# Optimization experiments

Measured on AMD Instinct MI355X. Metric: run time of the kernel, lower is better.

## Reference

```python
import jax, jax.numpy as jnp
import numpy as np

PRE_NMS_TOPN = 6000   # cfg.TEST.RPN_PRE_NMS_TOP_N
POST_NMS_TOPN = 1000  # cfg.TEST.RPN_POST_NMS_TOP_N
NMS_THRESH = 0.7      # cfg.TEST.RPN_NMS_THRESH
MIN_SIZE = 0.0        # cfg.TEST.RPN_MIN_SIZE
BBOX_XFORM_CLIP = float(np.log(1000.0 / 16.0))
FEAT_STRIDE = 8.0     # 1 / spatial_scale


def _generate_anchors(base_size=16, ratios=(0.5, 1.0, 2.0), scales=(2, 4, 8, 16, 32)):
    """Standard Detectron anchor generation -> (A, 4) = (15, 4)."""
    def whctrs(a):
        w = a[2] - a[0] + 1.0
        h = a[3] - a[1] + 1.0
        return w, h, a[0] + 0.5 * (w - 1.0), a[1] + 0.5 * (h - 1.0)

    def mk(ws, hs, xc, yc):
        ws = ws[:, None]; hs = hs[:, None]
        return np.hstack([xc - 0.5 * (ws - 1.0), yc - 0.5 * (hs - 1.0),
                          xc + 0.5 * (ws - 1.0), yc + 0.5 * (hs - 1.0)])

    base = np.array([0.0, 0.0, base_size - 1.0, base_size - 1.0])
    w, h, xc, yc = whctrs(base)
    rs = np.array(ratios)
    ws = np.round(np.sqrt(w * h / rs))
    hs = np.round(ws * rs)
    ratio_anchors = mk(ws, hs, xc, yc)
    out = []
    for a in ratio_anchors:
        w, h, xc, yc = whctrs(a)
        sc = np.array(scales, dtype=np.float64)
        out.append(mk(w * sc, h * sc, xc, yc))
    return np.vstack(out).astype(np.float32)


def _proposals_one_image(all_anchors, im_info, bbox_deltas, scores):
    # bbox_deltas: (4A, H, W), scores: (A, H, W)
    deltas = bbox_deltas.transpose(1, 2, 0).reshape(-1, 4)  # (K*A, 4)
    s = scores.transpose(1, 2, 0).reshape(-1)               # (K*A,)

    # pre-NMS top-k by objectness (argpartition+argsort in original)
    top_s, order = jax.lax.top_k(s, PRE_NMS_TOPN)
    d = deltas[order]
    anc = all_anchors[order]

    # bbox_transform with weights (1,1,1,1) and dw/dh clipping
    ws = anc[:, 2] - anc[:, 0] + 1.0
    hs = anc[:, 3] - anc[:, 1] + 1.0
    cx = anc[:, 0] + 0.5 * ws
    cy = anc[:, 1] + 0.5 * hs
    dx, dy = d[:, 0], d[:, 1]
    dw = jnp.minimum(d[:, 2], BBOX_XFORM_CLIP)
    dh = jnp.minimum(d[:, 3], BBOX_XFORM_CLIP)
    pcx = dx * ws + cx
    pcy = dy * hs + cy
    pw = jnp.exp(dw) * ws
    ph = jnp.exp(dh) * hs
    x1 = pcx - 0.5 * pw
    y1 = pcy - 0.5 * ph
    x2 = pcx + 0.5 * pw - 1.0
    y2 = pcy + 0.5 * ph - 1.0

    # clip_tiled_boxes to image extent
    h_im, w_im, scale = im_info[0], im_info[1], im_info[2]
    x1 = jnp.clip(x1, 0.0, w_im - 1.0)
    y1 = jnp.clip(y1, 0.0, h_im - 1.0)
    x2 = jnp.clip(x2, 0.0, w_im - 1.0)
    y2 = jnp.clip(y2, 0.0, h_im - 1.0)
    boxes = jnp.stack([x1, y1, x2, y2], axis=1)  # (PRE, 4)

    # _filter_boxes -> validity mask (replaces gather-by-keep)
    bws = x2 - x1 + 1.0
    bhs = y2 - y1 + 1.0
    min_sz = MIN_SIZE * scale
    valid = (bws >= min_sz) & (bhs >= min_sz) & ((x1 + bws / 2.0) < w_im) & ((y1 + bhs / 2.0) < h_im)

    # greedy NMS on score-sorted boxes (boxes already sorted descending)
    areas = bws * bhs
    ix1 = jnp.maximum(x1[:, None], x1[None, :])
    iy1 = jnp.maximum(y1[:, None], y1[None, :])
    ix2 = jnp.minimum(x2[:, None], x2[None, :])
    iy2 = jnp.minimum(y2[:, None], y2[None, :])
    inter = jnp.maximum(ix2 - ix1 + 1.0, 0.0) * jnp.maximum(iy2 - iy1 + 1.0, 0.0)
    iou = inter / (areas[:, None] + areas[None, :] - inter)

    later = jnp.arange(PRE_NMS_TOPN)

    def body(i, keep):
        sup = keep[i] & (iou[i] > NMS_THRESH) & (later > i)
        return keep & ~sup

    keep = jax.lax.fori_loop(0, PRE_NMS_TOPN, body, valid)

    # fixed-size output: top POST_NMS_TOPN surviving boxes, padded (score=-1, box=0)
    masked = jnp.where(keep, top_s, -1.0)
    out_s, idx = jax.lax.top_k(masked, POST_NMS_TOPN)
    pad = (out_s > -1.0).astype(boxes.dtype)
    out_b = boxes[idx] * pad[:, None]
    return out_b, out_s


def reference(rpn_cls_prob, rpn_bbox_pred, im_info, anchors):
    N, A, H, W = rpn_cls_prob.shape
    dt = rpn_bbox_pred.dtype
    shift_x = jnp.arange(W, dtype=dt) * FEAT_STRIDE
    shift_y = jnp.arange(H, dtype=dt) * FEAT_STRIDE
    # torch.meshgrid default 'ij' ordering (faithful to original)
    sx, sy = jnp.meshgrid(shift_x, shift_y, indexing='ij')  # (W, H)
    shifts = jnp.stack([sx.ravel(), sy.ravel(), sx.ravel(), sy.ravel()], axis=1)  # (K, 4)
    all_anchors = (anchors[None, :, :] + shifts[:, None, :]).reshape(-1, 4)  # (K*A, 4)

    boxes, probs = jax.vmap(_proposals_one_image, in_axes=(None, 0, 0, 0))(
        all_anchors, im_info, rpn_bbox_pred, rpn_cls_prob)
    batch_inds = jnp.broadcast_to(jnp.arange(N, dtype=boxes.dtype)[:, None, None],
                                  (N, POST_NMS_TOPN, 1))
    rois = jnp.concatenate([batch_inds, boxes], axis=-1).reshape(-1, 5)
    return rois, probs.reshape(-1)


def setup_inputs() -> dict:
    key = jax.random.key(0)
    k1, k2 = jax.random.split(key)
    N, A, H, W = 2, 15, 128, 128
    rpn_cls_prob = jax.random.uniform(k1, (N, A, H, W), dtype=jnp.float32)
    rpn_bbox_pred = jax.random.normal(k2, (N, 4 * A, H, W), dtype=jnp.float32) * 0.2
    im_info = jnp.tile(jnp.array([[1024.0, 1024.0, 1.0]], dtype=jnp.float32), (N, 1))
    anchors = jnp.asarray(_generate_anchors())
    return {"rpn_cls_prob": rpn_cls_prob, "rpn_bbox_pred": rpn_bbox_pred,
            "im_info": im_info, "anchors": anchors}
```

## Files before the change

### kernel.cpp

```cpp
#include <hip/hip_runtime.h>
#include <hip/hip_bf16.h>

#define A_NUM 15
#define HDIM 128
#define WDIM 128
#define HW (HDIM*WDIM)
#define PER_IMG (A_NUM*HW)
#define NIMG 2
#define PRE_N 6000
#define POST_N 1000
#define NBLK 94
#define NPAD (NBLK*64)
#define SORTN 8192
#define CHUNK4 4096
#define NBIN 16384
#define HPART 16
#define NLOADS 47

typedef unsigned long long ull;

#define META_OFF   0u
#define HIST_OFF   64u
#define SEL_OFF    131136u
#define BOX_OFF    262208u
#define VALIDW_OFF 550976u
#define MASK_OFF   553024u

__device__ __forceinline__ unsigned int f2ord(float f) {
    unsigned int u = __float_as_uint(f);
    return (u & 0x80000000u) ? ~u : (u | 0x80000000u);
}
__device__ __forceinline__ float ord2f(unsigned int u) {
    unsigned int s = (u & 0x80000000u) ? (u ^ 0x80000000u) : ~u;
    return __uint_as_float(s);
}
__device__ __forceinline__ ull readlane64(ull v, int l) {
    unsigned int lo = (unsigned int)__builtin_amdgcn_readlane((int)(unsigned int)v, l);
    unsigned int hi = (unsigned int)__builtin_amdgcn_readlane((int)(unsigned int)(v >> 32), l);
    return ((ull)hi << 32) | lo;
}

typedef const unsigned int __attribute__((address_space(1)))* gas_u32;
typedef unsigned int __attribute__((address_space(3)))* las_u32;

__device__ __forceinline__ void async_col(const ull* __restrict__ gcol, ull* lcol, int t) {
    #pragma unroll
    for (int q = 0; q < NLOADS; ++q) {
        __builtin_amdgcn_global_load_lds(
            (gas_u32)(const void*)((const char*)gcol + q * 1024 + t * 16),
            (las_u32)(void*)((char*)lcol + q * 1024 + t * 16),
            16, 0, 0);
    }
}

__global__ __launch_bounds__(1024) void k_hist16(const float* __restrict__ cls,
                                                 unsigned int* __restrict__ hist) {
    __shared__ unsigned int h[NBIN];
    int img = blockIdx.y, part = blockIdx.x;
    int t = threadIdx.x;
    for (int b = t; b < NBIN; b += 1024) h[b] = 0;
    __syncthreads();
    int base = img * PER_IMG + part * (PER_IMG / HPART);
    for (int e = t; e < PER_IMG / HPART; e += 1024) {
        unsigned int u = f2ord(cls[base + e]);
        unsigned int bin = (u >> 16) - 0x8000u;
        if (bin > (NBIN - 1)) bin = NBIN - 1;
        atomicAdd(&h[bin], 1u);
    }
    __syncthreads();
    unsigned int* hp = hist + (size_t)img * NBIN;
    for (int b = t; b < NBIN; b += 1024)
        if (h[b]) atomicAdd(&hp[b], h[b]);
}

__global__ __launch_bounds__(1024) void k_scan16(const unsigned int* __restrict__ hist,
                                                 unsigned int* __restrict__ meta) {
    __shared__ unsigned int csum[1024];
    __shared__ unsigned int aux[64];
    __shared__ unsigned int binv[16];
    int img = blockIdx.x, t = threadIdx.x;
    const unsigned int* hp = hist + (size_t)img * NBIN;
    unsigned int s = 0;
    #pragma unroll
    for (int q = 0; q < 16; ++q) s += hp[t * 16 + q];
    csum[t] = s;
    __syncthreads();
    if (t < 64) {
        unsigned int x = 0;
        #pragma unroll
        for (int q = 0; q < 16; ++q) x += csum[t * 16 + q];
        aux[t] = x;
    }
    __syncthreads();
    if (t < 64) {
        unsigned int suf = 0;
        for (int q = t; q < 64; ++q) suf += aux[q];
        ull mb1 = __ballot(suf >= PRE_N);
        int sstar = 63 - __clzll(mb1);
        unsigned int sufnext = (unsigned)__shfl((int)suf, (sstar + 1) & 63);
        unsigned int cumAbove = (sstar == 63) ? 0u : sufnext;
        unsigned int sufC = 0;
        if (t < 16) {
            for (int q = sstar * 16 + t; q < sstar * 16 + 16; ++q) sufC += csum[q];
            sufC += cumAbove;
        }
        ull mb2 = __ballot((t < 16) && (sufC >= PRE_N));
        int crel = 63 - __clzll(mb2);
        int cstar = sstar * 16 + crel;
        unsigned int cumAbove2 = (crel == 15) ? cumAbove : (unsigned)__shfl((int)sufC, crel + 1);
        if (t < 16) binv[t] = hp[cstar * 16 + t];
        unsigned int sufB = 0;
        if (t < 16) {
            for (int q = t; q < 16; ++q) sufB += binv[q];
            sufB += cumAbove2;
        }
        ull mb3 = __ballot((t < 16) && (sufB >= PRE_N));
        int brel = 63 - __clzll(mb3);
        if (t == 0) {
            meta[2 + img] = (unsigned)(cstar * 16 + brel) + 0x8000u;
            meta[img] = 0u;
        }
    }
}

__global__ __launch_bounds__(256) void k_gather(const float* __restrict__ cls,
                                                unsigned int* __restrict__ meta,
                                                ull* __restrict__ selkeys) {
    __shared__ unsigned int lcnt[NIMG], lbase[NIMG];
    int t = threadIdx.x;
    int tid = blockIdx.x * 256 + t;
    if (t < NIMG) lcnt[t] = 0;
    __syncthreads();
    unsigned int T0 = meta[2], T1 = meta[3];
    int a = tid / HW;
    int pos = tid - a * HW;
    int m = pos * A_NUM + a;
    int lane = t & 63;
    unsigned int uv[NIMG];
    bool pr[NIMG];
    unsigned int lofs[NIMG];
    #pragma unroll
    for (int img = 0; img < NIMG; ++img) {
        unsigned int T = img ? T1 : T0;
        unsigned int u = f2ord(cls[img * PER_IMG + tid]);
        uv[img] = u;
        bool pred = (u >> 16) >= T;
        pr[img] = pred;
        ull mball = __ballot((int)pred);
        unsigned int o = 0;
        if (pred) {
            int leader = __ffsll((long long)mball) - 1;
            unsigned int wbase = 0;
            if (lane == leader) wbase = atomicAdd(&lcnt[img], (unsigned)__popcll(mball));
            wbase = (unsigned)__shfl((int)wbase, leader);
            o = wbase + (unsigned)__popcll(mball & ((1ull << lane) - 1ull));
        }
        lofs[img] = o;
    }
    __syncthreads();
    if (t < NIMG) lbase[t] = atomicAdd(&meta[t], lcnt[t]);
    __syncthreads();
    #pragma unroll
    for (int img = 0; img < NIMG; ++img) {
        if (pr[img]) {
            unsigned int p = lbase[img] + lofs[img];
            if (p < SORTN)
                selkeys[(size_t)img * SORTN + p] =
                    ((ull)(~uv[img]) << 32) | (unsigned int)m;
        }
    }
}

__global__ __launch_bounds__(512) void k_sortA(ull* __restrict__ selkeys,
                                               const unsigned int* __restrict__ meta) {
    __shared__ ull key[CHUNK4];
    int img = blockIdx.x >> 1, c = blockIdx.x & 1;
    unsigned int cnt = meta[img];
    if (cnt > SORTN) cnt = SORTN;
    ull* g = selkeys + (size_t)img * SORTN;
    int base = c * CHUNK4;
    for (int i = threadIdx.x; i < CHUNK4; i += 512)
        key[i] = (base + i < (int)cnt) ? g[base + i] : ~0ull;
    __syncthreads();
    bool desc = (c & 1);
    for (int k = 2; k <= CHUNK4; k <<= 1) {
        for (int j = k >> 1; j > 0; j >>= 1) {
            for (int p = threadIdx.x; p < CHUNK4 / 2; p += 512) {
                int i = ((p & ~(j - 1)) << 1) | (p & (j - 1));
                int x = i | j;
                bool up = (((i & k) == 0) != desc);
                ull A = key[i], B = key[x];
                if ((A > B) == up) { key[i] = B; key[x] = A; }
            }
            __syncthreads();
        }
    }
    for (int i = threadIdx.x; i < CHUNK4; i += 512) g[base + i] = key[i];
}

__global__ __launch_bounds__(512) void k_sortC(ull* __restrict__ selkeys) {
    __shared__ ull key[SORTN];
    int img = blockIdx.x;
    ull* g = selkeys + (size_t)img * SORTN;
    for (int i = threadIdx.x; i < SORTN; i += 512) key[i] = g[i];
    __syncthreads();
    for (int j = SORTN / 2; j > 0; j >>= 1) {
        for (int p = threadIdx.x; p < SORTN / 2; p += 512) {
            int i = ((p & ~(j - 1)) << 1) | (p & (j - 1));
            int x = i | j;
            ull A = key[i], B = key[x];
            if (A > B) { key[i] = B; key[x] = A; }
        }
        __syncthreads();
    }
    for (int i = threadIdx.x; i < PRE_N; i += 512) g[i] = key[i];
}

__global__ void k_decode(const ull* __restrict__ selkeys,
                         const float* __restrict__ bbox, const float* __restrict__ anchors,
                         const float* __restrict__ iminfo,
                         float* __restrict__ boxsoa, ull* __restrict__ validwArr) {
    int r = blockIdx.x * blockDim.x + threadIdx.x;
    int img = blockIdx.y;
    bool in = r < PRE_N;
    int rr = in ? r : 0;
    ull keyv = selkeys[(size_t)img * SORTN + rr];
    unsigned int m = (unsigned int)(keyv & 0xFFFFFFFFu);
    unsigned int u = ~(unsigned int)(keyv >> 32);
    float score = ord2f(u);
    int q = m / A_NUM;
    int a = m - q * A_NUM;
    int w = q & (WDIM - 1);
    int h = q >> 7;
    float sx = (float)h * 8.0f;
    float sy = (float)w * 8.0f;
    float a0 = __fadd_rn(anchors[a * 4 + 0], sx);
    float a1 = __fadd_rn(anchors[a * 4 + 1], sy);
    float a2 = __fadd_rn(anchors[a * 4 + 2], sx);
    float a3 = __fadd_rn(anchors[a * 4 + 3], sy);
    float ws = __fadd_rn(__fsub_rn(a2, a0), 1.0f);
    float hs = __fadd_rn(__fsub_rn(a3, a1), 1.0f);
    float cx = __fadd_rn(a0, __fmul_rn(0.5f, ws));
    float cy = __fadd_rn(a1, __fmul_rn(0.5f, hs));
    const float* bb = bbox + (size_t)img * 4 * A_NUM * HW;
    int base = h * WDIM + w;
    float dx = bb[(a * 4 + 0) * HW + base];
    float dy = bb[(a * 4 + 1) * HW + base];
    float dwv = bb[(a * 4 + 2) * HW + base];
    float dhv = bb[(a * 4 + 3) * HW + base];
    const float CLIPV = 4.135166556742356f;
    float dw = fminf(dwv, CLIPV);
    float dh = fminf(dhv, CLIPV);
    float pcx = __fadd_rn(__fmul_rn(dx, ws), cx);
    float pcy = __fadd_rn(__fmul_rn(dy, hs), cy);
    float pw = __fmul_rn(expf(dw), ws);
    float ph = __fmul_rn(expf(dh), hs);
    float x1 = __fsub_rn(pcx, __fmul_rn(0.5f, pw));
    float y1 = __fsub_rn(pcy, __fmul_rn(0.5f, ph));
    float x2 = __fsub_rn(__fadd_rn(pcx, __fmul_rn(0.5f, pw)), 1.0f);
    float y2 = __fsub_rn(__fadd_rn(pcy, __fmul_rn(0.5f, ph)), 1.0f);
    float him = iminfo[img * 3 + 0], wim = iminfo[img * 3 + 1], scale = iminfo[img * 3 + 2];
    float wmax = __fsub_rn(wim, 1.0f), hmax = __fsub_rn(him, 1.0f);
    x1 = fminf(fmaxf(x1, 0.0f), wmax);
    y1 = fminf(fmaxf(y1, 0.0f), hmax);
    x2 = fminf(fmaxf(x2, 0.0f), wmax);
    y2 = fminf(fmaxf(y2, 0.0f), hmax);
    float bws = __fadd_rn(__fsub_rn(x2, x1), 1.0f);
    float bhs = __fadd_rn(__fsub_rn(y2, y1), 1.0f);
    float minsz = __fmul_rn(0.0f, scale);
    bool valid = (bws >= minsz) && (bhs >= minsz) &&
                 (__fadd_rn(x1, __fdiv_rn(bws, 2.0f)) < wim) &&
                 (__fadd_rn(y1, __fdiv_rn(bhs, 2.0f)) < him);
    float area = __fmul_rn(bws, bhs);
    if (in) {
        boxsoa[(0 * NIMG + img) * NPAD + r] = x1;
        boxsoa[(1 * NIMG + img) * NPAD + r] = y1;
        boxsoa[(2 * NIMG + img) * NPAD + r] = x2;
        boxsoa[(3 * NIMG + img) * NPAD + r] = y2;
        boxsoa[(4 * NIMG + img) * NPAD + r] = area;
        boxsoa[(5 * NIMG + img) * NPAD + r] = score;
    }
    ull bw = __ballot((int)(in && valid));
    if ((threadIdx.x & 63) == 0) {
        int blk = r >> 6;
        if (blk < NBLK) validwArr[img * 128 + blk] = bw;
    }
}

__global__ __launch_bounds__(256) void k_mask(const float* __restrict__ boxsoa,
                                              ull* __restrict__ Mc) {
    int cb = blockIdx.x, rbq = blockIdx.y, img = blockIdx.z;
    if ((rbq << 2) > cb) return;
    int t = threadIdx.x, wv = t >> 6, lane = t & 63;
    __shared__ float jx1[64], jy1[64], jx2[64], jy2[64], jar[64];
    const float* X1 = boxsoa + (0 * NIMG + img) * NPAD;
    const float* Y1 = boxsoa + (1 * NIMG + img) * NPAD;
    const float* X2 = boxsoa + (2 * NIMG + img) * NPAD;
    const float* Y2 = boxsoa + (3 * NIMG + img) * NPAD;
    const float* AR = boxsoa + (4 * NIMG + img) * NPAD;
    int j0 = cb * 64;
    if (t < 64) {
        int jidx = j0 + t;
        bool jin = jidx < PRE_N;
        jx1[t] = jin ? X1[jidx] : 0.0f;
        jy1[t] = jin ? Y1[jidx] : 0.0f;
        jx2[t] = jin ? X2[jidx] : 0.0f;
        jy2[t] = jin ? Y2[jidx] : 0.0f;
        jar[t] = jin ? AR[jidx] : 1.0f;
    }
    __syncthreads();
    int rb = rbq * 4 + wv;
    if (rb > cb) return;
    int r = rb * 64 + lane;
    ull bits = 0ULL;
    if (r < PRE_N) {
        float x1 = X1[r], y1 = Y1[r], x2 = X2[r], y2 = Y2[r], ai = AR[r];
        for (int jj = 0; jj < 64; ++jj) {
            int j = j0 + jj;
            if (j == r || j >= PRE_N) continue;
            float ix1 = fmaxf(x1, jx1[jj]);
            float iy1 = fmaxf(y1, jy1[jj]);
            float ix2 = fminf(x2, jx2[jj]);
            float iy2 = fminf(y2, jy2[jj]);
            float iw = fmaxf(__fadd_rn(__fsub_rn(ix2, ix1), 1.0f), 0.0f);
            float ih = fmaxf(__fadd_rn(__fsub_rn(iy2, iy1), 1.0f), 0.0f);
            float inter = __fmul_rn(iw, ih);
            float denom = __fsub_rn(__fadd_rn(ai, jar[jj]), inter);
            float iou = __fdiv_rn(inter, denom);
            if (iou > 0.7f) bits |= (1ULL << jj);
        }
    }
    Mc[((size_t)img * NBLK + cb) * NPAD + r] = bits;
}

__global__ __launch_bounds__(64, 1) void k_reduce(const ull* __restrict__ Mc,
                                                  const ull* __restrict__ validwArr,
                                                  const float* __restrict__ boxsoa,
                                                  float* __restrict__ out) {
    __shared__ ull buf[2][NPAD];
    __shared__ unsigned short s_list[POST_N];
    int img = blockIdx.x;
    int t = threadIdx.x;
    const ull* MC = Mc + (size_t)img * NBLK * NPAD;
    ull vw_a = validwArr[img * 128 + t];
    ull vw_b = (t + 64 < NBLK) ? validwArr[img * 128 + t + 64] : 0;
    async_col(MC, &buf[0][0], t);
    asm volatile("s_waitcnt vmcnt(0)" ::: "memory");
    __builtin_amdgcn_sched_barrier(0);
    ull d_cur = buf[0][t];
    async_col(MC + NPAD, &buf[1][0], t);
    ull kTlo = 0ULL, kThi = 0ULL;
    ull acc_cur = 0ULL;
    int cnt = 0;
    for (int ib = 0; ib < NBLK; ++ib) {
        if (ib + 2 < NBLK)
            async_col(MC + (size_t)(ib + 2) * NPAD, &buf[ib & 1][0], t);
        unsigned int lo = (unsigned)acc_cur, hi = (unsigned)(acc_cur >> 32);
        #pragma unroll
        for (int s2 = 1; s2 < 64; s2 <<= 1) {
            lo |= (unsigned)__shfl_xor((int)lo, s2);
            hi |= (unsigned)__shfl_xor((int)hi, s2);
        }
        ull sup = ((ull)hi << 32) | lo;
        ull validw = (ib < 64) ? readlane64(vw_a, ib) : readlane64(vw_b, ib - 64);
        ull live = validw & ~sup;
        unsigned int dlo = (unsigned)d_cur, dhi = (unsigned)(d_cur >> 32);
        ull keptb = 0ULL;
        while (live) {
            int b = __ffsll((long long)live) - 1;
            keptb |= 1ULL << b;
            if (t == 0) s_list[cnt] = (unsigned short)(ib * 64 + b);
            ++cnt;
            if (cnt >= POST_N) break;
            unsigned int rl = (unsigned)__builtin_amdgcn_readlane((int)dlo, b);
            unsigned int rh = (unsigned)__builtin_amdgcn_readlane((int)dhi, b);
            live &= ~(((ull)rh << 32) | rl);
            live &= ~(1ULL << b);
        }
        if (cnt >= POST_N) break;
        ull mybit = (keptb >> t) & 1ULL;
        if (ib < 64) kTlo |= mybit << ib;
        else kThi |= mybit << (ib - 64);
        if (ib + 1 < NBLK) {
            if (ib + 2 < NBLK) asm volatile("s_waitcnt vmcnt(47)" ::: "memory");
            else               asm volatile("s_waitcnt vmcnt(0)" ::: "memory");
            __builtin_amdgcn_sched_barrier(0);
            const ull* bn = &buf[(ib + 1) & 1][0];
            d_cur = bn[(ib + 1) * 64 + t];
            ull a0 = 0ULL, a1 = 0ULL, a2 = 0ULL, a3 = 0ULL;
            int u = 0;
            for (; u + 4 <= ib + 1; u += 4) {
                ull v0 = bn[(u + 0) * 64 + t];
                ull v1 = bn[(u + 1) * 64 + t];
                ull v2 = bn[(u + 2) * 64 + t];
                ull v3 = bn[(u + 3) * 64 + t];
                ull m0 = ((u + 0 < 64) ? (kTlo >> (u + 0)) : (kThi >> (u + 0 - 64))) & 1ULL;
                ull m1 = ((u + 1 < 64) ? (kTlo >> (u + 1)) : (kThi >> (u + 1 - 64))) & 1ULL;
                ull m2 = ((u + 2 < 64) ? (kTlo >> (u + 2)) : (kThi >> (u + 2 - 64))) & 1ULL;
                ull m3 = ((u + 3 < 64) ? (kTlo >> (u + 3)) : (kThi >> (u + 3 - 64))) & 1ULL;
                a0 |= (0ULL - m0) & v0;
                a1 |= (0ULL - m1) & v1;
                a2 |= (0ULL - m2) & v2;
                a3 |= (0ULL - m3) & v3;
            }
            for (; u <= ib; ++u) {
                ull v = bn[u * 64 + t];
                ull mm = ((u < 64) ? (kTlo >> u) : (kThi >> (u - 64))) & 1ULL;
                a0 |= (0ULL - mm) & v;
            }
            acc_cur = (a0 | a1) | (a2 | a3);
            asm volatile("s_waitcnt lgkmcnt(0)" ::: "memory");
            __builtin_amdgcn_sched_barrier(0);
        }
    }
    asm volatile("s_waitcnt vmcnt(0) lgkmcnt(0)" ::: "memory");
    __builtin_amdgcn_sched_barrier(0);
    int total = cnt > POST_N ? POST_N : cnt;
    for (int k = t; k < POST_N; k += 64) {
        float x1 = 0.0f, y1 = 0.0f, x2 = 0.0f, y2 = 0.0f, sc = -1.0f;
        if (k < total) {
            int r = (int)s_list[k];
            x1 = boxsoa[(0 * NIMG + img) * NPAD + r];
            y1 = boxsoa[(1 * NIMG + img) * NPAD + r];
            x2 = boxsoa[(2 * NIMG + img) * NPAD + r];
            y2 = boxsoa[(3 * NIMG + img) * NPAD + r];
            sc = boxsoa[(5 * NIMG + img) * NPAD + r];
        }
        float* roi = out + (size_t)(img * POST_N + k) * 5;
        roi[0] = (float)img;
        roi[1] = x1;
        roi[2] = y1;
        roi[3] = x2;
        roi[4] = y2;
        out[NIMG * POST_N * 5 + img * POST_N + k] = sc;
    }
}

extern "C" void kernel_launch(void* const* d_in, const int* in_sizes, int n_in,
                              void* d_out, int out_size, void* d_ws, size_t ws_size,
                              hipStream_t stream) {
    const float* cls = (const float*)d_in[0];
    const float* bbox = (const float*)d_in[1];
    const float* iminfo = (const float*)d_in[2];
    const float* anchors = (const float*)d_in[3];
    float* out = (float*)d_out;
    char* ws = (char*)d_ws;

    unsigned int* meta = (unsigned int*)(ws + META_OFF);
    unsigned int* hist = (unsigned int*)(ws + HIST_OFF);
    ull* selkeys = (ull*)(ws + SEL_OFF);
    float* boxsoa = (float*)(ws + BOX_OFF);
    ull* validwArr = (ull*)(ws + VALIDW_OFF);
    ull* mask = (ull*)(ws + MASK_OFF);

    hipMemsetAsync(hist, 0, (size_t)NIMG * NBIN * sizeof(unsigned int), stream);
    k_hist16<<<dim3(HPART, NIMG), 1024, 0, stream>>>(cls, hist);
    k_scan16<<<NIMG, 1024, 0, stream>>>(hist, meta);
    k_gather<<<PER_IMG / 256, 256, 0, stream>>>(cls, meta, selkeys);
    k_sortA<<<2 * NIMG, 512, 0, stream>>>(selkeys, meta);
    k_sortC<<<NIMG, 512, 0, stream>>>(selkeys);
    k_decode<<<dim3((PRE_N + 255) / 256, NIMG), 256, 0, stream>>>(selkeys, bbox, anchors, iminfo,
                                                                  boxsoa, validwArr);
    k_mask<<<dim3(NBLK, (NBLK + 3) / 4, NIMG), 256, 0, stream>>>(boxsoa, mask);
    k_reduce<<<NIMG, 64, 0, stream>>>(mask, validwArr, boxsoa, out);
}
```

Measured before the change: 283.8 us.

## Transpose NMS mask column layout with padded stride and fully unroll reduction

k_mask now writes each mask column in a transposed layout where each lane's row block entries are contiguous with a padded stride of 97, so k_reduce reads bn[t*TSTRIDE+u]. The padding is meant to avoid LDS bank conflicts. The inner OR-accumulation over kept blocks is fully unrolled over all 94 blocks with eight accumulators and no dynamic trip count, and the explicit lgkmcnt wait is removed. It trades extra LDS reads of unused (zero or stale) blocks for straight-line code. The async load count and vmcnt threshold change to match the larger column size.

```diff
diff --git a/kernel.cpp b/kernel.cpp
--- a/kernel.cpp
+++ b/kernel.cpp
@@ -15,7 +15,9 @@
 #define CHUNK4 4096
 #define NBIN 16384
 #define HPART 16
-#define NLOADS 47
+#define TSTRIDE 97
+#define COLW 6272
+#define NLOADS 49
 
 typedef unsigned long long ull;
 
@@ -288,7 +290,7 @@
 }
 
 __global__ __launch_bounds__(256) void k_mask(const float* __restrict__ boxsoa,
-                                              ull* __restrict__ Mc) {
+                                              ull* __restrict__ Mct) {
     int cb = blockIdx.x, rbq = blockIdx.y, img = blockIdx.z;
     if ((rbq << 2) > cb) return;
     int t = threadIdx.x, wv = t >> 6, lane = t & 63;
@@ -330,31 +332,31 @@
             if (iou > 0.7f) bits |= (1ULL << jj);
         }
     }
-    Mc[((size_t)img * NBLK + cb) * NPAD + r] = bits;
-}
-
-__global__ __launch_bounds__(64, 1) void k_reduce(const ull* __restrict__ Mc,
+    Mct[(size_t)(img * NBLK + cb) * COLW + lane * TSTRIDE + rb] = bits;
+}
+
+__global__ __launch_bounds__(64, 1) void k_reduce(const ull* __restrict__ Mct,
                                                   const ull* __restrict__ validwArr,
                                                   const float* __restrict__ boxsoa,
                                                   float* __restrict__ out) {
-    __shared__ ull buf[2][NPAD];
+    __shared__ ull buf[2][COLW];
     __shared__ unsigned short s_list[POST_N];
     int img = blockIdx.x;
     int t = threadIdx.x;
-    const ull* MC = Mc + (size_t)img * NBLK * NPAD;
+    const ull* MC = Mct + (size_t)img * NBLK * COLW;
     ull vw_a = validwArr[img * 128 + t];
     ull vw_b = (t + 64 < NBLK) ? validwArr[img * 128 + t + 64] : 0;
     async_col(MC, &buf[0][0], t);
     asm volatile("s_waitcnt vmcnt(0)" ::: "memory");
     __builtin_amdgcn_sched_barrier(0);
-    ull d_cur = buf[0][t];
-    async_col(MC + NPAD, &buf[1][0], t);
+    ull d_cur = buf[0][t * TSTRIDE];
+    async_col(MC + COLW, &buf[1][0], t);
     ull kTlo = 0ULL, kThi = 0ULL;
     ull acc_cur = 0ULL;
     int cnt = 0;
     for (int ib = 0; ib < NBLK; ++ib) {
         if (ib + 2 < NBLK)
-            async_col(MC + (size_t)(ib + 2) * NPAD, &buf[ib & 1][0], t);
+            async_col(MC + (size_t)(ib + 2) * COLW, &buf[ib & 1][0], t);
         unsigned int lo = (unsigned)acc_cur, hi = (unsigned)(acc_cur >> 32);
         #pragma unroll
         for (int s2 = 1; s2 < 64; s2 <<= 1) {
@@ -382,35 +384,20 @@
         if (ib < 64) kTlo |= mybit << ib;
         else kThi |= mybit << (ib - 64);
         if (ib + 1 < NBLK) {
-            if (ib + 2 < NBLK) asm volatile("s_waitcnt vmcnt(47)" ::: "memory");
+            if (ib + 2 < NBLK) asm volatile("s_waitcnt vmcnt(49)" ::: "memory");
             else               asm volatile("s_waitcnt vmcnt(0)" ::: "memory");
             __builtin_amdgcn_sched_barrier(0);
             const ull* bn = &buf[(ib + 1) & 1][0];
-            d_cur = bn[(ib + 1) * 64 + t];
-            ull a0 = 0ULL, a1 = 0ULL, a2 = 0ULL, a3 = 0ULL;
-            int u = 0;
-            for (; u + 4 <= ib + 1; u += 4) {
-                ull v0 = bn[(u + 0) * 64 + t];
-                ull v1 = bn[(u + 1) * 64 + t];
-                ull v2 = bn[(u + 2) * 64 + t];
-                ull v3 = bn[(u + 3) * 64 + t];
-                ull m0 = ((u + 0 < 64) ? (kTlo >> (u + 0)) : (kThi >> (u + 0 - 64))) & 1ULL;
-                ull m1 = ((u + 1 < 64) ? (kTlo >> (u + 1)) : (kThi >> (u + 1 - 64))) & 1ULL;
-                ull m2 = ((u + 2 < 64) ? (kTlo >> (u + 2)) : (kThi >> (u + 2 - 64))) & 1ULL;
-                ull m3 = ((u + 3 < 64) ? (kTlo >> (u + 3)) : (kThi >> (u + 3 - 64))) & 1ULL;
-                a0 |= (0ULL - m0) & v0;
-                a1 |= (0ULL - m1) & v1;
-                a2 |= (0ULL - m2) & v2;
-                a3 |= (0ULL - m3) & v3;
+            d_cur = bn[t * TSTRIDE + (ib + 1)];
+            ull a_[8] = {0ULL, 0ULL, 0ULL, 0ULL, 0ULL, 0ULL, 0ULL, 0ULL};
+            #pragma unroll
+            for (int u = 0; u < NBLK; ++u) {
+                ull v = bn[t * TSTRIDE + u];
+                ull mm = ((u < 64) ? (kTlo >> u) : (kThi >> (u - 64))) & 1ULL;
+                a_[u & 7] |= (0ULL - mm) & v;
             }
-            for (; u <= ib; ++u) {
-                ull v = bn[u * 64 + t];
-                ull mm = ((u < 64) ? (kTlo >> u) : (kThi >> (u - 64))) & 1ULL;
-                a0 |= (0ULL - mm) & v;
-            }
-            acc_cur = (a0 | a1) | (a2 | a3);
-            asm volatile("s_waitcnt lgkmcnt(0)" ::: "memory");
-            __builtin_amdgcn_sched_barrier(0);
+            acc_cur = ((a_[0] | a_[1]) | (a_[2] | a_[3])) |
+                      ((a_[4] | a_[5]) | (a_[6] | a_[7]));
         }
     }
     asm volatile("s_waitcnt vmcnt(0) lgkmcnt(0)" ::: "memory");
```

Measured after the change: 305.8 us. 1.08x slower.
